# Kernel optimization log

Measured on AMD Instinct MI355X. Metric: run time of the kernel, lower is better.

Reference implementation:

```python
import jax, jax.numpy as jnp
import numpy as np

SEQ_LEN, BATCH, NUM_GROUPS, GROUP = 12, 512, 16, 32
H, E, MLP, BOTTLE, PRE = 128, 64, 1024, 1024, 512


def _pool_net(h, pos, num_groups, Wp, bp, W1, b1, W2, b2):
    # PoolHiddenNet: for each scene group, pairwise relative positions -> MLP -> max over neighbors
    B = h.shape[0]
    G = B // num_groups
    hg = h.reshape(num_groups, G, -1)          # (NG, G, H)
    pg = pos.reshape(num_groups, G, 2)         # (NG, G, 2)
    rel = pg[:, None, :, :] - pg[:, :, None, :]  # [g,i,j] = pos_j - pos_i
    emb = rel @ Wp.T + bp                      # (NG, G, G, E)
    hj = jnp.broadcast_to(hg[:, None, :, :], (num_groups, G, G, hg.shape[-1]))
    feats = jnp.concatenate([emb, hj], axis=-1)  # (NG, G, G, E+H)
    x = jax.nn.relu(feats @ W1.T + b1)         # (NG, G, G, 512)
    x = jax.nn.relu(x @ W2.T + b2)             # (NG, G, G, 1024)
    return x.max(axis=2).reshape(B, -1)        # max over neighbors j


def setup_inputs() -> dict:
    key = jax.random.key(0)
    ks = jax.random.split(key, 24)
    s = 0.05
    starts = np.arange(NUM_GROUPS, dtype=np.int64) * GROUP
    seq_start_end = jnp.asarray(np.stack([starts, starts + GROUP], axis=1))
    return {
        "last_pos": jax.random.normal(ks[0], (BATCH, 2), jnp.float32),
        "last_pos_rel": jax.random.normal(ks[1], (BATCH, 2), jnp.float32),
        "hh": jax.random.normal(ks[2], (1, BATCH, H), jnp.float32),
        "ch": jax.random.normal(ks[3], (1, BATCH, H), jnp.float32),
        "pred_traj_rel": jax.random.normal(ks[4], (SEQ_LEN, BATCH, 2), jnp.float32),
        "seq_start_end": seq_start_end,
        # LSTM (torch layout: gates ordered i,f,g,o)
        "W_ih": jax.random.normal(ks[5], (4 * H, E), jnp.float32) * s,
        "W_hh": jax.random.normal(ks[6], (4 * H, H), jnp.float32) * s,
        "b_ih": jax.random.normal(ks[7], (4 * H,), jnp.float32) * s,
        "b_hh": jax.random.normal(ks[8], (4 * H,), jnp.float32) * s,
        # spatial_embedding Linear(2, E)
        "Wse": jax.random.normal(ks[9], (E, 2), jnp.float32) * s,
        "bse": jax.random.normal(ks[10], (E,), jnp.float32) * s,
        # hidden2pos Linear(H, 2)
        "Wpos": jax.random.normal(ks[11], (2, H), jnp.float32) * s,
        "bpos": jax.random.normal(ks[12], (2,), jnp.float32) * s,
        # pool_net spatial_embedding Linear(2, E)
        "Wp": jax.random.normal(ks[13], (E, 2), jnp.float32) * s,
        "bp": jax.random.normal(ks[14], (E,), jnp.float32) * s,
        # pool_net mlp_pre_pool: [E+H, 512, BOTTLE], relu after each linear
        "W1": jax.random.normal(ks[15], (PRE, E + H), jnp.float32) * s,
        "b1": jax.random.normal(ks[16], (PRE,), jnp.float32) * s,
        "W2": jax.random.normal(ks[17], (BOTTLE, PRE), jnp.float32) * s,
        "b2": jax.random.normal(ks[18], (BOTTLE,), jnp.float32) * s,
        # decoder mlp: [H+BOTTLE, MLP, H], relu after each linear
        "Wm1": jax.random.normal(ks[19], (MLP, H + BOTTLE), jnp.float32) * s,
        "bm1": jax.random.normal(ks[20], (MLP,), jnp.float32) * s,
        "Wm2": jax.random.normal(ks[21], (H, MLP), jnp.float32) * s,
        "bm2": jax.random.normal(ks[22], (H,), jnp.float32) * s,
    }


def reference(last_pos, last_pos_rel, hh, ch, pred_traj_rel, seq_start_end,
              W_ih, W_hh, b_ih, b_hh, Wse, bse, Wpos, bpos,
              Wp, bp, W1, b1, W2, b2, Wm1, bm1, Wm2, bm2):
    num_groups = seq_start_end.shape[0]
    h0, c0 = hh[0], ch[0]
    dec_in0 = last_pos_rel @ Wse.T + bse

    def step(carry, gt_rel):
        last_pos_c, h, c, dec_in, loss = carry
        # single-layer LSTM cell (torch gate order i,f,g,o)
        gates = dec_in @ W_ih.T + b_ih + h @ W_hh.T + b_hh
        i, f, g, o = jnp.split(gates, 4, axis=-1)
        c = jax.nn.sigmoid(f) * c + jax.nn.sigmoid(i) * jnp.tanh(g)
        h = jax.nn.sigmoid(o) * jnp.tanh(c)
        rel_pos = h @ Wpos.T + bpos
        curr_pos = rel_pos + last_pos_c
        # pool every timestep + mlp back down to h_dim, replaces hidden state
        pool_h = _pool_net(h, curr_pos, num_groups, Wp, bp, W1, b1, W2, b2)
        dh = jnp.concatenate([h, pool_h], axis=1)
        dh = jax.nn.relu(dh @ Wm1.T + bm1)
        h = jax.nn.relu(dh @ Wm2.T + bm2)
        # training mode: teacher forcing + MSE loss
        loss = loss + jnp.mean((rel_pos - gt_rel) ** 2)
        dec_in = gt_rel @ Wse.T + bse
        return (curr_pos, h, c, dec_in, loss), rel_pos

    init = (last_pos, h0, c0, dec_in0, jnp.float32(0.0))
    (_, _, _, _, loss), pred_traj = jax.lax.scan(step, init, pred_traj_rel)
    return pred_traj, loss
```

## Files before the change

kernel.cpp:

```cpp
#include <hip/hip_runtime.h>
#include <math.h>

#define BATCH 512
#define NG 16
#define GSZ 32
#define H 128
#define E 64
#define PRE 512
#define BOT 1024
#define MLPD 1024
#define SEQ 12
#define AK 1152

typedef __attribute__((ext_vector_type(8))) short bf16x8;
typedef __attribute__((ext_vector_type(4))) float f32x4;

union bf8pack { ushort s[8]; uint4 v; };

__device__ __forceinline__ unsigned short f2bf(float f) {
    unsigned u = __float_as_uint(f);
    u += 0x7FFF + ((u >> 16) & 1);
    return (unsigned short)(u >> 16);
}
__device__ __forceinline__ float bf2f(unsigned short s) {
    return __uint_as_float(((unsigned)s) << 16);
}

#define GLB(p) ((const __attribute__((address_space(1))) unsigned int*)(p))
#define LDS(p) ((__attribute__((address_space(3))) unsigned int*)(p))

#define N0 (BOT * PRE)
#define N1 (MLPD * AK)
#define N2 (H * MLPD)
#define N3 (PRE * H)
#define N4 (PRE)
#define N5 (BATCH * H)
#define N5b (BATCH * H)
#define N6 (BATCH * 2)
#define N7 (512 * 128)
#define N8 (512)
#define PREP_TOT (N0 + N1 + N2 + N3 + N4 + N5 + N5b + N6 + N7 + N8 + 1)

__global__ void prep_kernel(
    const float* __restrict__ W2, const float* __restrict__ Wm1,
    const float* __restrict__ Wm2, const float* __restrict__ W1,
    const float* __restrict__ Wp, const float* __restrict__ bp, const float* __restrict__ b1,
    const float* __restrict__ ch, const float* __restrict__ hh, const float* __restrict__ last_pos,
    const float* __restrict__ Wih, const float* __restrict__ Whh,
    const float* __restrict__ bih, const float* __restrict__ bhh,
    const float* __restrict__ Wse, const float* __restrict__ bse,
    unsigned short* __restrict__ W2pk, unsigned short* __restrict__ Wm1pk,
    unsigned short* __restrict__ Wm2pk, unsigned short* __restrict__ W1pk,
    float* __restrict__ Wcx, float* __restrict__ Wcy, float* __restrict__ biash,
    float* __restrict__ cbuf, float* __restrict__ hbuf, float* __restrict__ pos,
    unsigned short* __restrict__ Whpk,
    float* __restrict__ Wx0, float* __restrict__ Wx1, float* __restrict__ bx,
    float* __restrict__ loss)
{
    long idx = (long)blockIdx.x * 256 + threadIdx.x;
    if (idx < N0) {
        int e = (int)(idx & 7);
        long u = idx >> 3;
        int lane = (int)(u & 63);
        int rest = (int)(u >> 6);
        int ksg = rest & 15, cg = rest >> 4;
        int col = cg * 16 + (lane & 15);
        int kk = ksg * 32 + (lane >> 4) * 8 + e;
        W2pk[idx] = f2bf(W2[(size_t)col * PRE + kk]);
        return;
    }
    idx -= N0;
    if (idx < N1) {
        int e = (int)(idx & 7);
        long u = idx >> 3;
        int lane = (int)(u & 63);
        long rest = u >> 6;
        int ksg = (int)(rest % 36);
        int cg = (int)(rest / 36);
        int col = cg * 16 + (lane & 15);
        int k = ksg * 32 + (lane >> 4) * 8 + e;
        Wm1pk[idx] = f2bf(Wm1[(size_t)col * AK + k]);
        return;
    }
    idx -= N1;
    if (idx < N2) {
        int e = (int)(idx & 7);
        long u = idx >> 3;
        int lane = (int)(u & 63);
        int rest = (int)(u >> 6);
        int ksg = rest & 31, cg = rest >> 5;
        int col = cg * 16 + (lane & 15);
        int k = ksg * 32 + (lane >> 4) * 8 + e;
        Wm2pk[idx] = f2bf(Wm2[(size_t)col * MLPD + k]);
        return;
    }
    idx -= N2;
    if (idx < N3) {
        int e = (int)(idx & 7);
        int u = (int)(idx >> 3);
        int l16 = u & 15, quad = (u >> 4) & 3, nt = (u >> 6) & 3, ks = (u >> 8) & 3, w = u >> 10;
        int col = w * 64 + nt * 16 + l16;
        int k = ks * 32 + quad * 8 + e;
        W1pk[idx] = f2bf(W1[col * 192 + E + k]);
        return;
    }
    idx -= N3;
    if (idx < N4) {
        int p = (int)idx;
        float sx = 0.f, sy = 0.f, sb = 0.f;
#pragma unroll 8
        for (int e = 0; e < E; ++e) {
            float w = W1[p * 192 + e];
            sx += w * Wp[e * 2 + 0];
            sy += w * Wp[e * 2 + 1];
            sb += w * bp[e];
        }
        Wcx[p] = sx; Wcy[p] = sy; biash[p] = b1[p] + sb;
        return;
    }
    idx -= N4;
    if (idx < N5) { cbuf[idx] = ch[idx]; return; }
    idx -= N5;
    if (idx < N5b) { hbuf[idx] = hh[idx]; return; }
    idx -= N5b;
    if (idx < N6) { pos[idx] = last_pos[idx]; return; }
    idx -= N6;
    if (idx < N7) {
        int e = (int)(idx & 7);
        int u = (int)(idx >> 3);
        int l16 = u & 15, quad = (u >> 4) & 3, ks = (u >> 6) & 3, w = (u >> 8) & 7, g = u >> 11;
        int col = g * 128 + w * 16 + l16;
        int k = ks * 32 + quad * 8 + e;
        Whpk[idx] = f2bf(Whh[col * H + k]);
        return;
    }
    idx -= N7;
    if (idx < N8) {
        int u = (int)idx;
        float sx = 0.f, sy = 0.f, sb = 0.f;
#pragma unroll 8
        for (int e = 0; e < E; ++e) {
            float w = Wih[u * E + e];
            sx += w * Wse[e * 2 + 0];
            sy += w * Wse[e * 2 + 1];
            sb += w * bse[e];
        }
        Wx0[u] = sx; Wx1[u] = sy; bx[u] = sb + bih[u] + bhh[u];
        return;
    }
    idx -= N8;
    if (idx == 0) *loss = 0.0f;
}

#define LROWS 16
__global__ __launch_bounds__(512) void lstm_hpart(
    int t,
    const float* __restrict__ relin, const float* __restrict__ gt,
    const unsigned short* __restrict__ Whpk,
    const float* __restrict__ Wx0, const float* __restrict__ Wx1, const float* __restrict__ bx,
    const float* __restrict__ Wpos, const float* __restrict__ bpos,
    const unsigned short* __restrict__ W1pk, const float* __restrict__ biash,
    const float* __restrict__ hbuf, float* __restrict__ cbuf,
    unsigned short* __restrict__ Abf, float* __restrict__ Hpartf,
    float* __restrict__ pos, float* __restrict__ traj, float* __restrict__ loss)
{
    constexpr int LDHB = 136;
    constexpr int LDHF = 129;
    __shared__ __align__(16) unsigned short As[LROWS * LDHB];
    __shared__ __align__(16) unsigned short hnb[LROWS * LDHB];
    __shared__ float hnf[LROWS * LDHF];
    __shared__ float lred[8];
    const int r0 = blockIdx.x * LROWS;
    const int tid = threadIdx.x;
    const int lane = tid & 63, w = tid >> 6;
    const int quad = lane >> 4, l16 = lane & 15;

    for (int idx = tid; idx < LROWS * H; idx += 512) {
        int row = idx >> 7, k = idx & 127;
        As[row * LDHB + k] = f2bf(hbuf[(size_t)(r0 + row) * H + k]);
    }
    __syncthreads();

    f32x4 acc[4];
#pragma unroll
    for (int g4 = 0; g4 < 4; ++g4) acc[g4] = (f32x4)0.f;
#pragma unroll
    for (int ks = 0; ks < 4; ++ks) {
        bf16x8 af = *(const bf16x8*)&As[l16 * LDHB + ks * 32 + quad * 8];
#pragma unroll
        for (int gate = 0; gate < 4; ++gate) {
            bf16x8 bf = *(const bf16x8*)&Whpk[((size_t)((gate * 8 + w) * 4 + ks) * 64 + lane) * 8];
            acc[gate] = __builtin_amdgcn_mfma_f32_16x16x32_bf16(af, bf, acc[gate], 0, 0, 0);
        }
    }

    {
        int u = w * 16 + l16;
        float wx0[4], wx1[4], bxv[4];
#pragma unroll
        for (int gate = 0; gate < 4; ++gate) {
            int col = gate * 128 + u;
            wx0[gate] = Wx0[col]; wx1[gate] = Wx1[col]; bxv[gate] = bx[col];
        }
#pragma unroll
        for (int r = 0; r < 4; ++r) {
            int row = quad * 4 + r;
            int b = r0 + row;
            float rx = relin[b * 2 + 0], ry = relin[b * 2 + 1];
            float i_ = acc[0][r] + rx * wx0[0] + ry * wx1[0] + bxv[0];
            float f_ = acc[1][r] + rx * wx0[1] + ry * wx1[1] + bxv[1];
            float g_ = acc[2][r] + rx * wx0[2] + ry * wx1[2] + bxv[2];
            float o_ = acc[3][r] + rx * wx0[3] + ry * wx1[3] + bxv[3];
            float ig = 1.0f / (1.0f + expf(-i_));
            float fg = 1.0f / (1.0f + expf(-f_));
            float gg = tanhf(g_);
            float og = 1.0f / (1.0f + expf(-o_));
            float c = fg * cbuf[(size_t)b * H + u] + ig * gg;
            cbuf[(size_t)b * H + u] = c;
            float h = og * tanhf(c);
            hnb[row * LDHB + u] = f2bf(h);
            hnf[row * LDHF + u] = h;
            Abf[(size_t)b * AK + u] = f2bf(h);
        }
    }
    __syncthreads();

    if (t < SEQ - 1) {
        f32x4 acc2[4];
#pragma unroll
        for (int nt = 0; nt < 4; ++nt) acc2[nt] = (f32x4)0.f;
#pragma unroll
        for (int ks = 0; ks < 4; ++ks) {
            bf16x8 af = *(const bf16x8*)&hnb[l16 * LDHB + ks * 32 + quad * 8];
#pragma unroll
            for (int nt = 0; nt < 4; ++nt) {
                bf16x8 bfr = *(const bf16x8*)&W1pk[((size_t)((w * 4 + ks) * 4 + nt) * 64 + lane) * 8];
                acc2[nt] = __builtin_amdgcn_mfma_f32_16x16x32_bf16(af, bfr, acc2[nt], 0, 0, 0);
            }
        }
#pragma unroll
        for (int nt = 0; nt < 4; ++nt) {
            int col = w * 64 + nt * 16 + l16;
            float bv = biash[col];
#pragma unroll
            for (int r = 0; r < 4; ++r) {
                int row = quad * 4 + r;
                Hpartf[(size_t)(r0 + row) * PRE + col] = acc2[nt][r] + bv;
            }
        }
    }

    {
        int row = tid >> 5, o = (tid >> 4) & 1, seg = tid & 15;
        const float* wr = Wpos + o * H + seg * 8;
        const float* hr = &hnf[row * LDHF + seg * 8];
        float acc3 = 0.f;
#pragma unroll
        for (int k = 0; k < 8; ++k) acc3 += wr[k] * hr[k];
        acc3 += __shfl_xor(acc3, 1);
        acc3 += __shfl_xor(acc3, 2);
        acc3 += __shfl_xor(acc3, 4);
        acc3 += __shfl_xor(acc3, 8);
        acc3 += bpos[o];
        int b = r0 + row;
        float d = acc3 - gt[b * 2 + o];
        if (seg == 0) {
            float lp = pos[b * 2 + o];
            pos[b * 2 + o] = acc3 + lp;
            traj[b * 2 + o] = acc3;
        }
        float part = (seg == 0) ? d * d : 0.f;
        part += __shfl_xor(part, 16);
        part += __shfl_xor(part, 32);
        if (lane == 0) lred[w] = part;
        __syncthreads();
        if (tid == 0) {
            float s = 0.f;
#pragma unroll
            for (int i = 0; i < 8; ++i) s += lred[i];
            atomicAdd(loss, s * (1.0f / 1024.0f));
        }
    }
}

template <int BM, int BN, int KW, int NW, int MODE>
__global__ __launch_bounds__(256) void gemm_splitk_pk(
    const unsigned short* __restrict__ A, int lda,
    const unsigned short* __restrict__ Bpk, int K,
    const float* __restrict__ bias,
    float* __restrict__ Cf, unsigned short* __restrict__ Cb, int ldc)
{
    constexpr int MT = BM / 16;
    constexpr int NT = BN / (16 * NW);
    __shared__ __align__(16) unsigned short As[KW * BM * 64];
    __shared__ float red[KW * BM * BN];
    int tid = threadIdx.x;
    int lane = tid & 63, w = tid >> 6;
    int kslice = w / NW, nslice = w % NW;
    int gtid = tid & (NW * 64 - 1);
    int quad = lane >> 4, l16 = lane & 15;
    int m0 = blockIdx.y * BM, n0 = blockIdx.x * BN;
    const int KC = K / KW;
    const int KSGT = K >> 5;
    const int cgbase = (n0 + nslice * (BN / NW)) >> 4;

    f32x4 acc[MT][NT];
#pragma unroll
    for (int mt = 0; mt < MT; ++mt)
#pragma unroll
        for (int nt = 0; nt < NT; ++nt) acc[mt][nt] = (f32x4)0.f;

    for (int k0 = 0; k0 < KC; k0 += 64) {
        int kb = kslice * KC + k0;
        int kgbase = kb >> 5;
#pragma unroll
        for (int u = 0; u < BM / (8 * NW); ++u) {
            int c = u * NW * 64 + gtid;
            __builtin_amdgcn_global_load_lds(
                GLB(A + (size_t)(m0 + (c >> 3)) * lda + kb + (c & 7) * 8),
                LDS(&As[kslice * BM * 64 + c * 8]), 16, 0, 0);
        }
        __syncthreads();
#pragma unroll
        for (int ks = 0; ks < 2; ++ks) {
            bf16x8 af[MT], bfr[NT];
#pragma unroll
            for (int mt = 0; mt < MT; ++mt)
                af[mt] = *(const bf16x8*)&As[kslice * BM * 64 + (mt * 16 + l16) * 64 + ks * 32 + quad * 8];
#pragma unroll
            for (int nt = 0; nt < NT; ++nt)
                bfr[nt] = *(const bf16x8*)&Bpk[((size_t)((cgbase + nt) * KSGT + kgbase + ks) * 64 + lane) * 8];
#pragma unroll
            for (int mt = 0; mt < MT; ++mt)
#pragma unroll
                for (int nt = 0; nt < NT; ++nt)
                    acc[mt][nt] = __builtin_amdgcn_mfma_f32_16x16x32_bf16(af[mt], bfr[nt], acc[mt][nt], 0, 0, 0);
        }
        __syncthreads();
    }

#pragma unroll
    for (int mt = 0; mt < MT; ++mt)
#pragma unroll
    for (int nt = 0; nt < NT; ++nt) {
#pragma unroll
        for (int r = 0; r < 4; ++r) {
            int row = mt * 16 + quad * 4 + r;
            int col = nslice * (BN / NW) + nt * 16 + l16;
            red[kslice * BM * BN + row * BN + col] = acc[mt][nt][r];
        }
    }
    __syncthreads();

#pragma unroll
    for (int o = 0; o < BM * BN / 256; ++o) {
        int e = o * 256 + tid;
        int row = e / BN, col = e % BN;
        float s = 0.f;
#pragma unroll
        for (int k = 0; k < KW; ++k) s += red[k * BM * BN + e];
        float v = fmaxf(s + bias[n0 + col], 0.f);
        if (MODE == 1) Cb[(size_t)(m0 + row) * ldc + n0 + col] = f2bf(v);
        else           Cf[(size_t)(m0 + row) * ldc + n0 + col] = v;
    }
}

__global__ __launch_bounds__(512) void pool_fused(
    const float* __restrict__ Hpartf, const float* __restrict__ pos,
    const float* __restrict__ Wcx, const float* __restrict__ Wcy,
    const unsigned short* __restrict__ W2pk,
    const float* __restrict__ b2, unsigned short* __restrict__ Abf)
{
    constexpr int BN = 512;
    constexpr int LDA = 72;
    __shared__ __align__(16) unsigned short As[128 * LDA];
    const int tid = threadIdx.x;
    const int lane = tid & 63, w = tid >> 6;
    const int quad = lane >> 4, l16 = lane & 15;
    const int n_tile = blockIdx.x, m_tile = blockIdx.y;
    const int g = m_tile >> 3, iq = m_tile & 7;
    const int n0 = n_tile * BN;

    const int brow = tid >> 2;
    const int k8 = (tid & 3) * 16;
    const int bi = iq * 4 + (brow >> 5), bj = brow & 31;
    const float rx = pos[(g * GSZ + bj) * 2 + 0] - pos[(g * GSZ + bi) * 2 + 0];
    const float ry = pos[(g * GSZ + bj) * 2 + 1] - pos[(g * GSZ + bi) * 2 + 1];
    const float* hrow = &Hpartf[(size_t)(g * GSZ + bj) * PRE];

    f32x4 acc[8][4];
#pragma unroll
    for (int mt = 0; mt < 8; ++mt)
#pragma unroll
        for (int nt = 0; nt < 4; ++nt) acc[mt][nt] = (f32x4)0.f;

    for (int k0i = 0; k0i < 8; ++k0i) {
        const int k0 = k0i * 64;
        {
            const float4* hp = (const float4*)(hrow + k0 + k8);
            const float4* wx = (const float4*)(Wcx + k0 + k8);
            const float4* wy = (const float4*)(Wcy + k0 + k8);
            bf8pack o[2];
#pragma unroll
            for (int q = 0; q < 2; ++q) {
                float4 ha = hp[q * 2], hb = hp[q * 2 + 1];
                float4 xa = wx[q * 2], xb = wx[q * 2 + 1];
                float4 ya = wy[q * 2], yb = wy[q * 2 + 1];
                o[q].s[0] = f2bf(fmaxf(ha.x + rx * xa.x + ry * ya.x, 0.f));
                o[q].s[1] = f2bf(fmaxf(ha.y + rx * xa.y + ry * ya.y, 0.f));
                o[q].s[2] = f2bf(fmaxf(ha.z + rx * xa.z + ry * ya.z, 0.f));
                o[q].s[3] = f2bf(fmaxf(ha.w + rx * xa.w + ry * ya.w, 0.f));
                o[q].s[4] = f2bf(fmaxf(hb.x + rx * xb.x + ry * yb.x, 0.f));
                o[q].s[5] = f2bf(fmaxf(hb.y + rx * xb.y + ry * yb.y, 0.f));
                o[q].s[6] = f2bf(fmaxf(hb.z + rx * xb.z + ry * yb.z, 0.f));
                o[q].s[7] = f2bf(fmaxf(hb.w + rx * xb.w + ry * yb.w, 0.f));
            }
            *(uint4*)&As[brow * LDA + k8] = o[0].v;
            *(uint4*)&As[brow * LDA + k8 + 8] = o[1].v;
        }
        __syncthreads();
#pragma unroll
        for (int ks = 0; ks < 2; ++ks) {
            bf16x8 bfr[4];
#pragma unroll
            for (int nt = 0; nt < 4; ++nt) {
                int cg = n_tile * 32 + w * 4 + nt;
                int ksg = k0i * 2 + ks;
                bfr[nt] = *(const bf16x8*)&W2pk[((size_t)(cg * 16 + ksg) * 64 + lane) * 8];
            }
#pragma unroll
            for (int mt = 0; mt < 8; ++mt) {
                bf16x8 af = *(const bf16x8*)&As[(mt * 16 + l16) * LDA + ks * 32 + quad * 8];
#pragma unroll
                for (int nt = 0; nt < 4; ++nt)
                    acc[mt][nt] = __builtin_amdgcn_mfma_f32_16x16x32_bf16(af, bfr[nt], acc[mt][nt], 0, 0, 0);
            }
        }
        __syncthreads();
    }

#pragma unroll
    for (int il = 0; il < 4; ++il)
#pragma unroll
    for (int nt = 0; nt < 4; ++nt) {
        float u = -1e30f;
#pragma unroll
        for (int p = 0; p < 2; ++p)
#pragma unroll
            for (int r = 0; r < 4; ++r) u = fmaxf(u, acc[il * 2 + p][nt][r]);
        u = fmaxf(u, __shfl_xor(u, 16));
        u = fmaxf(u, __shfl_xor(u, 32));
        if (lane < 16) {
            int col = n0 + w * 64 + nt * 16 + l16;
            int gu = m_tile * 4 + il;
            Abf[(size_t)gu * AK + H + col] = f2bf(fmaxf(u + b2[col], 0.f));
        }
    }
}

extern "C" void kernel_launch(void* const* d_in, const int* in_sizes, int n_in,
                              void* d_out, int out_size, void* d_ws, size_t ws_size,
                              hipStream_t stream)
{
    const float* last_pos     = (const float*)d_in[0];
    const float* last_pos_rel = (const float*)d_in[1];
    const float* hh           = (const float*)d_in[2];
    const float* ch           = (const float*)d_in[3];
    const float* ptr_rel      = (const float*)d_in[4];
    const float* Wih  = (const float*)d_in[6];
    const float* Whh  = (const float*)d_in[7];
    const float* bih  = (const float*)d_in[8];
    const float* bhh  = (const float*)d_in[9];
    const float* Wse  = (const float*)d_in[10];
    const float* bse  = (const float*)d_in[11];
    const float* Wpos = (const float*)d_in[12];
    const float* bpos = (const float*)d_in[13];
    const float* Wp   = (const float*)d_in[14];
    const float* bp   = (const float*)d_in[15];
    const float* W1   = (const float*)d_in[16];
    const float* b1   = (const float*)d_in[17];
    const float* W2   = (const float*)d_in[18];
    const float* b2   = (const float*)d_in[19];
    const float* Wm1  = (const float*)d_in[20];
    const float* bm1  = (const float*)d_in[21];
    const float* Wm2  = (const float*)d_in[22];
    const float* bm2  = (const float*)d_in[23];

    float* ws     = (float*)d_ws;
    float* hbuf   = ws;
    float* cbuf   = hbuf + BATCH * H;
    float* pos    = cbuf + BATCH * H;
    float* Hpartf = pos + 1024;
    float* Wcx    = Hpartf + BATCH * PRE;
    float* Wcy    = Wcx + PRE;
    float* biash  = Wcy + PRE;
    float* bx     = biash + PRE;
    float* Wx0    = bx + 512;
    float* Wx1    = Wx0 + 512;
    unsigned short* ub    = (unsigned short*)(Wx1 + 512);
    unsigned short* Abf   = ub;
    unsigned short* dhbf  = Abf + (size_t)BATCH * AK;
    unsigned short* W2pk  = dhbf + (size_t)BATCH * MLPD;
    unsigned short* Wm1pk = W2pk + (size_t)BOT * PRE;
    unsigned short* Wm2pk = Wm1pk + (size_t)MLPD * AK;
    unsigned short* W1pk  = Wm2pk + (size_t)H * MLPD;
    unsigned short* Whpk  = W1pk + (size_t)PRE * H;

    float* out  = (float*)d_out;
    float* loss = out + SEQ * BATCH * 2;

    prep_kernel<<<(PREP_TOT + 255) / 256, 256, 0, stream>>>(
        W2, Wm1, Wm2, W1, Wp, bp, b1, ch, hh, last_pos, Wih, Whh, bih, bhh, Wse, bse,
        W2pk, Wm1pk, Wm2pk, W1pk, Wcx, Wcy, biash, cbuf, hbuf, pos, Whpk, Wx0, Wx1, bx, loss);

    for (int t = 0; t < SEQ; t++) {
        const float* relin = (t == 0) ? last_pos_rel : (ptr_rel + (t - 1) * BATCH * 2);
        const float* gt = ptr_rel + t * BATCH * 2;
        lstm_hpart<<<BATCH / LROWS, 512, 0, stream>>>(t, relin, gt, Whpk, Wx0, Wx1, bx,
                                                      Wpos, bpos, W1pk, biash, hbuf, cbuf,
                                                      Abf, Hpartf, pos,
                                                      out + t * BATCH * 2, loss);
        if (t == SEQ - 1) break;
        pool_fused<<<dim3(2, 128), 512, 0, stream>>>(Hpartf, pos, Wcx, Wcy, W2pk, b2, Abf);
        gemm_splitk_pk<64, 32, 2, 2, 1><<<dim3(MLPD / 32, BATCH / 64), 256, 0, stream>>>(
            Abf, AK, Wm1pk, AK, bm1, nullptr, dhbf, MLPD);
        gemm_splitk_pk<16, 32, 4, 1, 2><<<dim3(H / 32, BATCH / 16), 256, 0, stream>>>(
            dhbf, MLPD, Wm2pk, MLPD, bm2, hbuf, nullptr, H);
    }
}
```

Baseline: 714.7 us.

## Merge per-timestep decoder kernels into one persistent kernel with grid barriers

The 45 per-timestep launches (LSTM, pooling, two MLP GEMMs) are replaced by a single persistent kernel of 256 blocks that loops over the timesteps. Stages are separated by a software grid barrier built on an atomic counter in global memory. The aim is to remove kernel launch overhead and inter-kernel gaps. In exchange, the LSTM stage now runs on only 32 of the 256 blocks while the rest wait at the barrier, and correctness depends on all 256 blocks being co-resident.

```diff
diff --git a/kernel.cpp b/kernel.cpp
--- a/kernel.cpp
+++ b/kernel.cpp
@@ -11,6 +11,7 @@
 #define MLPD 1024
 #define SEQ 12
 #define AK 1152
+#define NBLK 256
 
 typedef __attribute__((ext_vector_type(8))) short bf16x8;
 typedef __attribute__((ext_vector_type(4))) float f32x4;
@@ -21,9 +22,6 @@
     unsigned u = __float_as_uint(f);
     u += 0x7FFF + ((u >> 16) & 1);
     return (unsigned short)(u >> 16);
-}
-__device__ __forceinline__ float bf2f(unsigned short s) {
-    return __uint_as_float(((unsigned)s) << 16);
 }
 
 #define GLB(p) ((const __attribute__((address_space(1))) unsigned int*)(p))
@@ -39,7 +37,7 @@
 #define N6 (BATCH * 2)
 #define N7 (512 * 128)
 #define N8 (512)
-#define PREP_TOT (N0 + N1 + N2 + N3 + N4 + N5 + N5b + N6 + N7 + N8 + 1)
+#define PREP_TOT (N0 + N1 + N2 + N3 + N4 + N5 + N5b + N6 + N7 + N8 + 2)
 
 __global__ void prep_kernel(
     const float* __restrict__ W2, const float* __restrict__ Wm1,
@@ -55,7 +53,7 @@
     float* __restrict__ cbuf, float* __restrict__ hbuf, float* __restrict__ pos,
     unsigned short* __restrict__ Whpk,
     float* __restrict__ Wx0, float* __restrict__ Wx1, float* __restrict__ bx,
-    float* __restrict__ loss)
+    float* __restrict__ loss, unsigned* __restrict__ barcnt)
 {
     long idx = (long)blockIdx.x * 256 + threadIdx.x;
     if (idx < N0) {
@@ -149,312 +147,382 @@
         return;
     }
     idx -= N8;
-    if (idx == 0) *loss = 0.0f;
+    if (idx == 0) { *loss = 0.0f; return; }
+    if (idx == 1) { *barcnt = 0u; return; }
 }
 
+__device__ __forceinline__ void gsync(unsigned* cnt, unsigned target) {
+    __syncthreads();
+    if (threadIdx.x == 0) {
+        __threadfence();
+        atomicAdd(cnt, 1u);
+        while (__hip_atomic_load(cnt, __ATOMIC_RELAXED, __HIP_MEMORY_SCOPE_AGENT) < target)
+            __builtin_amdgcn_s_sleep(16);
+        __threadfence();
+    }
+    __syncthreads();
+}
+
 #define LROWS 16
-__global__ __launch_bounds__(512) void lstm_hpart(
-    int t,
-    const float* __restrict__ relin, const float* __restrict__ gt,
+__global__ __launch_bounds__(512, 2) void decoder_persistent(
+    const float* __restrict__ last_pos_rel, const float* __restrict__ ptr_rel,
     const unsigned short* __restrict__ Whpk,
     const float* __restrict__ Wx0, const float* __restrict__ Wx1, const float* __restrict__ bx,
     const float* __restrict__ Wpos, const float* __restrict__ bpos,
     const unsigned short* __restrict__ W1pk, const float* __restrict__ biash,
-    const float* __restrict__ hbuf, float* __restrict__ cbuf,
+    const float* __restrict__ Wcx, const float* __restrict__ Wcy,
+    const unsigned short* __restrict__ W2pk, const float* __restrict__ b2,
+    const unsigned short* __restrict__ Wm1pk, const float* __restrict__ bm1,
+    const unsigned short* __restrict__ Wm2pk, const float* __restrict__ bm2,
+    float* __restrict__ hbuf, float* __restrict__ cbuf,
     unsigned short* __restrict__ Abf, float* __restrict__ Hpartf,
-    float* __restrict__ pos, float* __restrict__ traj, float* __restrict__ loss)
+    unsigned short* __restrict__ dhbf,
+    float* __restrict__ pos, float* __restrict__ out, float* __restrict__ loss,
+    unsigned* __restrict__ barcnt)
 {
-    constexpr int LDHB = 136;
-    constexpr int LDHF = 129;
-    __shared__ __align__(16) unsigned short As[LROWS * LDHB];
-    __shared__ __align__(16) unsigned short hnb[LROWS * LDHB];
-    __shared__ float hnf[LROWS * LDHF];
-    __shared__ float lred[8];
-    const int r0 = blockIdx.x * LROWS;
-    const int tid = threadIdx.x;
+    __shared__ __align__(16) unsigned char smem[32768];
+    const int blk = blockIdx.x, tid = threadIdx.x;
     const int lane = tid & 63, w = tid >> 6;
     const int quad = lane >> 4, l16 = lane & 15;
-
-    for (int idx = tid; idx < LROWS * H; idx += 512) {
-        int row = idx >> 7, k = idx & 127;
-        As[row * LDHB + k] = f2bf(hbuf[(size_t)(r0 + row) * H + k]);
-    }
-    __syncthreads();
-
-    f32x4 acc[4];
-#pragma unroll
-    for (int g4 = 0; g4 < 4; ++g4) acc[g4] = (f32x4)0.f;
-#pragma unroll
-    for (int ks = 0; ks < 4; ++ks) {
-        bf16x8 af = *(const bf16x8*)&As[l16 * LDHB + ks * 32 + quad * 8];
-#pragma unroll
-        for (int gate = 0; gate < 4; ++gate) {
-            bf16x8 bf = *(const bf16x8*)&Whpk[((size_t)((gate * 8 + w) * 4 + ks) * 64 + lane) * 8];
-            acc[gate] = __builtin_amdgcn_mfma_f32_16x16x32_bf16(af, bf, acc[gate], 0, 0, 0);
+    unsigned phase = 0;
+
+    for (int t = 0; t < SEQ; ++t) {
+        if (blk < 32) {
+            constexpr int LDHB = 136;
+            constexpr int LDHF = 129;
+            unsigned short* As = (unsigned short*)smem;
+            unsigned short* hnb = As + LROWS * LDHB;
+            float* hnf = (float*)(hnb + LROWS * LDHB);
+            float* lred = hnf + LROWS * LDHF;
+            const int r0 = blk * LROWS;
+            const float* relin = (t == 0) ? last_pos_rel : (ptr_rel + (t - 1) * BATCH * 2);
+            const float* gt = ptr_rel + t * BATCH * 2;
+            float* traj = out + t * BATCH * 2;
+
+            for (int e2 = tid; e2 < LROWS * H; e2 += 512) {
+                int row = e2 >> 7, k = e2 & 127;
+                As[row * LDHB + k] = f2bf(hbuf[(size_t)(r0 + row) * H + k]);
+            }
+            __syncthreads();
+
+            f32x4 acc[4];
+#pragma unroll
+            for (int g4 = 0; g4 < 4; ++g4) acc[g4] = (f32x4)0.f;
+#pragma unroll
+            for (int ks = 0; ks < 4; ++ks) {
+                bf16x8 af = *(const bf16x8*)&As[l16 * LDHB + ks * 32 + quad * 8];
+#pragma unroll
+                for (int gate = 0; gate < 4; ++gate) {
+                    bf16x8 bf = *(const bf16x8*)&Whpk[((size_t)((gate * 8 + w) * 4 + ks) * 64 + lane) * 8];
+                    acc[gate] = __builtin_amdgcn_mfma_f32_16x16x32_bf16(af, bf, acc[gate], 0, 0, 0);
+                }
+            }
+
+            {
+                int u = w * 16 + l16;
+                float wx0[4], wx1[4], bxv[4];
+#pragma unroll
+                for (int gate = 0; gate < 4; ++gate) {
+                    int col = gate * 128 + u;
+                    wx0[gate] = Wx0[col]; wx1[gate] = Wx1[col]; bxv[gate] = bx[col];
+                }
+#pragma unroll
+                for (int r = 0; r < 4; ++r) {
+                    int row = quad * 4 + r;
+                    int b = r0 + row;
+                    float rx = relin[b * 2 + 0], ry = relin[b * 2 + 1];
+                    float i_ = acc[0][r] + rx * wx0[0] + ry * wx1[0] + bxv[0];
+                    float f_ = acc[1][r] + rx * wx0[1] + ry * wx1[1] + bxv[1];
+                    float g_ = acc[2][r] + rx * wx0[2] + ry * wx1[2] + bxv[2];
+                    float o_ = acc[3][r] + rx * wx0[3] + ry * wx1[3] + bxv[3];
+                    float ig = 1.0f / (1.0f + expf(-i_));
+                    float fg = 1.0f / (1.0f + expf(-f_));
+                    float gg = tanhf(g_);
+                    float og = 1.0f / (1.0f + expf(-o_));
+                    float c = fg * cbuf[(size_t)b * H + u] + ig * gg;
+                    cbuf[(size_t)b * H + u] = c;
+                    float h = og * tanhf(c);
+                    hnb[row * LDHB + u] = f2bf(h);
+                    hnf[row * LDHF + u] = h;
+                    Abf[(size_t)b * AK + u] = f2bf(h);
+                }
+            }
+            __syncthreads();
+
+            if (t < SEQ - 1) {
+                f32x4 acc2[4];
+#pragma unroll
+                for (int nt = 0; nt < 4; ++nt) acc2[nt] = (f32x4)0.f;
+#pragma unroll
+                for (int ks = 0; ks < 4; ++ks) {
+                    bf16x8 af = *(const bf16x8*)&hnb[l16 * LDHB + ks * 32 + quad * 8];
+#pragma unroll
+                    for (int nt = 0; nt < 4; ++nt) {
+                        bf16x8 bfr = *(const bf16x8*)&W1pk[((size_t)((w * 4 + ks) * 4 + nt) * 64 + lane) * 8];
+                        acc2[nt] = __builtin_amdgcn_mfma_f32_16x16x32_bf16(af, bfr, acc2[nt], 0, 0, 0);
+                    }
+                }
+#pragma unroll
+                for (int nt = 0; nt < 4; ++nt) {
+                    int col = w * 64 + nt * 16 + l16;
+                    float bv = biash[col];
+#pragma unroll
+                    for (int r = 0; r < 4; ++r) {
+                        int row = quad * 4 + r;
+                        Hpartf[(size_t)(r0 + row) * PRE + col] = acc2[nt][r] + bv;
+                    }
+                }
+            }
+
+            {
+                int row = tid >> 5, o = (tid >> 4) & 1, seg = tid & 15;
+                const float* wr = Wpos + o * H + seg * 8;
+                const float* hr = &hnf[row * LDHF + seg * 8];
+                float acc3 = 0.f;
+#pragma unroll
+                for (int k = 0; k < 8; ++k) acc3 += wr[k] * hr[k];
+                acc3 += __shfl_xor(acc3, 1);
+                acc3 += __shfl_xor(acc3, 2);
+                acc3 += __shfl_xor(acc3, 4);
+                acc3 += __shfl_xor(acc3, 8);
+                acc3 += bpos[o];
+                int b = r0 + row;
+                float d = acc3 - gt[b * 2 + o];
+                if (seg == 0) {
+                    float lp = pos[b * 2 + o];
+                    pos[b * 2 + o] = acc3 + lp;
+                    traj[b * 2 + o] = acc3;
+                }
+                float part = (seg == 0) ? d * d : 0.f;
+                part += __shfl_xor(part, 16);
+                part += __shfl_xor(part, 32);
+                if (lane == 0) lred[w] = part;
+                __syncthreads();
+                if (tid == 0) {
+                    float s = 0.f;
+#pragma unroll
+                    for (int i = 0; i < 8; ++i) s += lred[i];
+                    atomicAdd(loss, s * (1.0f / 1024.0f));
+                }
+            }
         }
-    }
-
-    {
-        int u = w * 16 + l16;
-        float wx0[4], wx1[4], bxv[4];
-#pragma unroll
-        for (int gate = 0; gate < 4; ++gate) {
-            int col = gate * 128 + u;
-            wx0[gate] = Wx0[col]; wx1[gate] = Wx1[col]; bxv[gate] = bx[col];
+        if (t == SEQ - 1) break;
+        ++phase; gsync(barcnt, phase * NBLK);
+
+        {
+            constexpr int LDA = 72;
+            unsigned short* AsP = (unsigned short*)smem;
+            const int n_tile = blk & 1, m_tile = blk >> 1;
+            const int g = m_tile >> 3, iq = m_tile & 7;
+            const int n0 = n_tile * 512;
+            const int brow = tid >> 2;
+            const int k8 = (tid & 3) * 16;
+            const int bi = iq * 4 + (brow >> 5), bj = brow & 31;
+            const float rx = pos[(g * GSZ + bj) * 2 + 0] - pos[(g * GSZ + bi) * 2 + 0];
+            const float ry = pos[(g * GSZ + bj) * 2 + 1] - pos[(g * GSZ + bi) * 2 + 1];
+            const float* hrow = &Hpartf[(size_t)(g * GSZ + bj) * PRE];
+
+            f32x4 acc[8][4];
+#pragma unroll
+            for (int mt = 0; mt < 8; ++mt)
+#pragma unroll
+                for (int nt = 0; nt < 4; ++nt) acc[mt][nt] = (f32x4)0.f;
+
+            for (int k0i = 0; k0i < 8; ++k0i) {
+                const int k0 = k0i * 64;
+                {
+                    const float4* hp = (const float4*)(hrow + k0 + k8);
+                    const float4* wx = (const float4*)(Wcx + k0 + k8);
+                    const float4* wy = (const float4*)(Wcy + k0 + k8);
+                    bf8pack o[2];
+#pragma unroll
+                    for (int q = 0; q < 2; ++q) {
+                        float4 ha = hp[q * 2], hb = hp[q * 2 + 1];
+                        float4 xa = wx[q * 2], xb = wx[q * 2 + 1];
+                        float4 ya = wy[q * 2], yb = wy[q * 2 + 1];
+                        o[q].s[0] = f2bf(fmaxf(ha.x + rx * xa.x + ry * ya.x, 0.f));
+                        o[q].s[1] = f2bf(fmaxf(ha.y + rx * xa.y + ry * ya.y, 0.f));
+                        o[q].s[2] = f2bf(fmaxf(ha.z + rx * xa.z + ry * ya.z, 0.f));
+                        o[q].s[3] = f2bf(fmaxf(ha.w + rx * xa.w + ry * ya.w, 0.f));
+                        o[q].s[4] = f2bf(fmaxf(hb.x + rx * xb.x + ry * yb.x, 0.f));
+                        o[q].s[5] = f2bf(fmaxf(hb.y + rx * xb.y + ry * yb.y, 0.f));
+                        o[q].s[6] = f2bf(fmaxf(hb.z + rx * xb.z + ry * yb.z, 0.f));
+                        o[q].s[7] = f2bf(fmaxf(hb.w + rx * xb.w + ry * yb.w, 0.f));
+                    }
+                    *(uint4*)&AsP[brow * LDA + k8] = o[0].v;
+                    *(uint4*)&AsP[brow * LDA + k8 + 8] = o[1].v;
+                }
+                __syncthreads();
+#pragma unroll
+                for (int ks = 0; ks < 2; ++ks) {
+                    bf16x8 bfr[4];
+#pragma unroll
+                    for (int nt = 0; nt < 4; ++nt) {
+                        int cg = n_tile * 32 + w * 4 + nt;
+                        int ksg = k0i * 2 + ks;
+                        bfr[nt] = *(const bf16x8*)&W2pk[((size_t)(cg * 16 + ksg) * 64 + lane) * 8];
+                    }
+#pragma unroll
+                    for (int mt = 0; mt < 8; ++mt) {
+                        bf16x8 af = *(const bf16x8*)&AsP[(mt * 16 + l16) * LDA + ks * 32 + quad * 8];
+#pragma unroll
+                        for (int nt = 0; nt < 4; ++nt)
+                            acc[mt][nt] = __builtin_amdgcn_mfma_f32_16x16x32_bf16(af, bfr[nt], acc[mt][nt], 0, 0, 0);
+                    }
+                }
+                __syncthreads();
+            }
+
+#pragma unroll
+            for (int il = 0; il < 4; ++il)
+#pragma unroll
+            for (int nt = 0; nt < 4; ++nt) {
+                float u = -1e30f;
+#pragma unroll
+                for (int p = 0; p < 2; ++p)
+#pragma unroll
+                    for (int r = 0; r < 4; ++r) u = fmaxf(u, acc[il * 2 + p][nt][r]);
+                u = fmaxf(u, __shfl_xor(u, 16));
+                u = fmaxf(u, __shfl_xor(u, 32));
+                if (lane < 16) {
+                    int col = n0 + w * 64 + nt * 16 + l16;
+                    int gu = m_tile * 4 + il;
+                    Abf[(size_t)gu * AK + H + col] = f2bf(fmaxf(u + b2[col], 0.f));
+                }
+            }
         }
-#pragma unroll
-        for (int r = 0; r < 4; ++r) {
-            int row = quad * 4 + r;
-            int b = r0 + row;
-            float rx = relin[b * 2 + 0], ry = relin[b * 2 + 1];
-            float i_ = acc[0][r] + rx * wx0[0] + ry * wx1[0] + bxv[0];
-            float f_ = acc[1][r] + rx * wx0[1] + ry * wx1[1] + bxv[1];
-            float g_ = acc[2][r] + rx * wx0[2] + ry * wx1[2] + bxv[2];
-            float o_ = acc[3][r] + rx * wx0[3] + ry * wx1[3] + bxv[3];
-            float ig = 1.0f / (1.0f + expf(-i_));
-            float fg = 1.0f / (1.0f + expf(-f_));
-            float gg = tanhf(g_);
-            float og = 1.0f / (1.0f + expf(-o_));
-            float c = fg * cbuf[(size_t)b * H + u] + ig * gg;
-            cbuf[(size_t)b * H + u] = c;
-            float h = og * tanhf(c);
-            hnb[row * LDHB + u] = f2bf(h);
-            hnf[row * LDHF + u] = h;
-            Abf[(size_t)b * AK + u] = f2bf(h);
+        ++phase; gsync(barcnt, phase * NBLK);
+
+        {
+            const int n0 = (blk & 31) * 32, m0 = (blk >> 5) * 64;
+            const bool act = tid < 256;
+            unsigned short* AsM = (unsigned short*)smem;
+            float* red = (float*)(smem + 16384);
+            const int w4 = (tid >> 6) & 3;
+            const int kslice = w4 >> 1, nslice = w4 & 1;
+            const int gtid = tid & 127;
+            const int cgbase = n0 / 16 + nslice;
+
+            f32x4 acc[4];
+#pragma unroll
+            for (int mt = 0; mt < 4; ++mt) acc[mt] = (f32x4)0.f;
+
+            for (int k0 = 0; k0 < 576; k0 += 64) {
+                int kb = kslice * 576 + k0;
+                int kgbase = kb >> 5;
+                if (act) {
+#pragma unroll
+                    for (int u = 0; u < 4; ++u) {
+                        int c = u * 128 + gtid;
+                        __builtin_amdgcn_global_load_lds(
+                            GLB(Abf + (size_t)(m0 + (c >> 3)) * AK + kb + (c & 7) * 8),
+                            LDS(&AsM[kslice * 4096 + c * 8]), 16, 0, 0);
+                    }
+                }
+                __syncthreads();
+                if (act) {
+#pragma unroll
+                    for (int ks = 0; ks < 2; ++ks) {
+                        bf16x8 af[4];
+#pragma unroll
+                        for (int mt = 0; mt < 4; ++mt)
+                            af[mt] = *(const bf16x8*)&AsM[kslice * 4096 + (mt * 16 + l16) * 64 + ks * 32 + quad * 8];
+                        bf16x8 bfr = *(const bf16x8*)&Wm1pk[((size_t)(cgbase * 36 + kgbase + ks) * 64 + lane) * 8];
+#pragma unroll
+                        for (int mt = 0; mt < 4; ++mt)
+                            acc[mt] = __builtin_amdgcn_mfma_f32_16x16x32_bf16(af[mt], bfr, acc[mt], 0, 0, 0);
+                    }
+                }
+                __syncthreads();
+            }
+
+            if (act) {
+#pragma unroll
+                for (int mt = 0; mt < 4; ++mt)
+#pragma unroll
+                for (int r = 0; r < 4; ++r) {
+                    int row = mt * 16 + quad * 4 + r;
+                    int col = nslice * 16 + l16;
+                    red[kslice * 2048 + row * 32 + col] = acc[mt][r];
+                }
+            }
+            __syncthreads();
+            if (act) {
+#pragma unroll
+                for (int o = 0; o < 8; ++o) {
+                    int e = o * 256 + tid;
+                    int row = e >> 5, col = e & 31;
+                    float s = red[e] + red[2048 + e];
+                    float v = fmaxf(s + bm1[n0 + col], 0.f);
+                    dhbf[(size_t)(m0 + row) * MLPD + n0 + col] = f2bf(v);
+                }
+            }
         }
-    }
-    __syncthreads();
-
-    if (t < SEQ - 1) {
-        f32x4 acc2[4];
-#pragma unroll
-        for (int nt = 0; nt < 4; ++nt) acc2[nt] = (f32x4)0.f;
-#pragma unroll
-        for (int ks = 0; ks < 4; ++ks) {
-            bf16x8 af = *(const bf16x8*)&hnb[l16 * LDHB + ks * 32 + quad * 8];
-#pragma unroll
-            for (int nt = 0; nt < 4; ++nt) {
-                bf16x8 bfr = *(const bf16x8*)&W1pk[((size_t)((w * 4 + ks) * 4 + nt) * 64 + lane) * 8];
-                acc2[nt] = __builtin_amdgcn_mfma_f32_16x16x32_bf16(af, bfr, acc2[nt], 0, 0, 0);
+        ++phase; gsync(barcnt, phase * NBLK);
+
+        if (blk < 128) {
+            const int n0 = (blk & 3) * 32, m0 = (blk >> 2) * 16;
+            const bool act = tid < 256;
+            unsigned short* As2 = (unsigned short*)smem;
+            float* red2 = (float*)(smem + 8192);
+            const int w4 = (tid >> 6) & 3;
+            const int gtid2 = tid & 63;
+            const int cgbase = n0 >> 4;
+
+            f32x4 acc[2];
+#pragma unroll
+            for (int nt = 0; nt < 2; ++nt) acc[nt] = (f32x4)0.f;
+
+            for (int k0 = 0; k0 < 256; k0 += 64) {
+                int kb = w4 * 256 + k0;
+                int kgbase = kb >> 5;
+                if (act) {
+#pragma unroll
+                    for (int u = 0; u < 2; ++u) {
+                        int c = u * 64 + gtid2;
+                        __builtin_amdgcn_global_load_lds(
+                            GLB(dhbf + (size_t)(m0 + (c >> 3)) * MLPD + kb + (c & 7) * 8),
+                            LDS(&As2[w4 * 1024 + c * 8]), 16, 0, 0);
+                    }
+                }
+                __syncthreads();
+                if (act) {
+#pragma unroll
+                    for (int ks = 0; ks < 2; ++ks) {
+                        bf16x8 af = *(const bf16x8*)&As2[w4 * 1024 + l16 * 64 + ks * 32 + quad * 8];
+#pragma unroll
+                        for (int nt = 0; nt < 2; ++nt) {
+                            bf16x8 bfr = *(const bf16x8*)&Wm2pk[((size_t)((cgbase + nt) * 32 + kgbase + ks) * 64 + lane) * 8];
+                            acc[nt] = __builtin_amdgcn_mfma_f32_16x16x32_bf16(af, bfr, acc[nt], 0, 0, 0);
+                        }
+                    }
+                }
+                __syncthreads();
+            }
+
+            if (act) {
+#pragma unroll
+                for (int nt = 0; nt < 2; ++nt)
+#pragma unroll
+                for (int r = 0; r < 4; ++r) {
+                    int row = quad * 4 + r;
+                    int col = nt * 16 + l16;
+                    red2[w4 * 512 + row * 32 + col] = acc[nt][r];
+                }
+            }
+            __syncthreads();
+            if (act) {
+#pragma unroll
+                for (int o = 0; o < 2; ++o) {
+                    int e = o * 256 + tid;
+                    int row = e >> 5, col = e & 31;
+                    float s = red2[e] + red2[512 + e] + red2[1024 + e] + red2[1536 + e];
+                    float v = fmaxf(s + bm2[n0 + col], 0.f);
+                    hbuf[(size_t)(m0 + row) * H + n0 + col] = v;
+                }
             }
         }
-#pragma unroll
-        for (int nt = 0; nt < 4; ++nt) {
-            int col = w * 64 + nt * 16 + l16;
-            float bv = biash[col];
-#pragma unroll
-            for (int r = 0; r < 4; ++r) {
-                int row = quad * 4 + r;
-                Hpartf[(size_t)(r0 + row) * PRE + col] = acc2[nt][r] + bv;
-            }
-        }
-    }
-
-    {
-        int row = tid >> 5, o = (tid >> 4) & 1, seg = tid & 15;
-        const float* wr = Wpos + o * H + seg * 8;
-        const float* hr = &hnf[row * LDHF + seg * 8];
-        float acc3 = 0.f;
-#pragma unroll
-        for (int k = 0; k < 8; ++k) acc3 += wr[k] * hr[k];
-        acc3 += __shfl_xor(acc3, 1);
-        acc3 += __shfl_xor(acc3, 2);
-        acc3 += __shfl_xor(acc3, 4);
-        acc3 += __shfl_xor(acc3, 8);
-        acc3 += bpos[o];
-        int b = r0 + row;
-        float d = acc3 - gt[b * 2 + o];
-        if (seg == 0) {
-            float lp = pos[b * 2 + o];
-            pos[b * 2 + o] = acc3 + lp;
-            traj[b * 2 + o] = acc3;
-        }
-        float part = (seg == 0) ? d * d : 0.f;
-        part += __shfl_xor(part, 16);
-        part += __shfl_xor(part, 32);
-        if (lane == 0) lred[w] = part;
-        __syncthreads();
-        if (tid == 0) {
-            float s = 0.f;
-#pragma unroll
-            for (int i = 0; i < 8; ++i) s += lred[i];
-            atomicAdd(loss, s * (1.0f / 1024.0f));
-        }
-    }
-}
-
-template <int BM, int BN, int KW, int NW, int MODE>
-__global__ __launch_bounds__(256) void gemm_splitk_pk(
-    const unsigned short* __restrict__ A, int lda,
-    const unsigned short* __restrict__ Bpk, int K,
-    const float* __restrict__ bias,
-    float* __restrict__ Cf, unsigned short* __restrict__ Cb, int ldc)
-{
-    constexpr int MT = BM / 16;
-    constexpr int NT = BN / (16 * NW);
-    __shared__ __align__(16) unsigned short As[KW * BM * 64];
-    __shared__ float red[KW * BM * BN];
-    int tid = threadIdx.x;
-    int lane = tid & 63, w = tid >> 6;
-    int kslice = w / NW, nslice = w % NW;
-    int gtid = tid & (NW * 64 - 1);
-    int quad = lane >> 4, l16 = lane & 15;
-    int m0 = blockIdx.y * BM, n0 = blockIdx.x * BN;
-    const int KC = K / KW;
-    const int KSGT = K >> 5;
-    const int cgbase = (n0 + nslice * (BN / NW)) >> 4;
-
-    f32x4 acc[MT][NT];
-#pragma unroll
-    for (int mt = 0; mt < MT; ++mt)
-#pragma unroll
-        for (int nt = 0; nt < NT; ++nt) acc[mt][nt] = (f32x4)0.f;
-
-    for (int k0 = 0; k0 < KC; k0 += 64) {
-        int kb = kslice * KC + k0;
-        int kgbase = kb >> 5;
-#pragma unroll
-        for (int u = 0; u < BM / (8 * NW); ++u) {
-            int c = u * NW * 64 + gtid;
-            __builtin_amdgcn_global_load_lds(
-                GLB(A + (size_t)(m0 + (c >> 3)) * lda + kb + (c & 7) * 8),
-                LDS(&As[kslice * BM * 64 + c * 8]), 16, 0, 0);
-        }
-        __syncthreads();
-#pragma unroll
-        for (int ks = 0; ks < 2; ++ks) {
-            bf16x8 af[MT], bfr[NT];
-#pragma unroll
-            for (int mt = 0; mt < MT; ++mt)
-                af[mt] = *(const bf16x8*)&As[kslice * BM * 64 + (mt * 16 + l16) * 64 + ks * 32 + quad * 8];
-#pragma unroll
-            for (int nt = 0; nt < NT; ++nt)
-                bfr[nt] = *(const bf16x8*)&Bpk[((size_t)((cgbase + nt) * KSGT + kgbase + ks) * 64 + lane) * 8];
-#pragma unroll
-            for (int mt = 0; mt < MT; ++mt)
-#pragma unroll
-                for (int nt = 0; nt < NT; ++nt)
-                    acc[mt][nt] = __builtin_amdgcn_mfma_f32_16x16x32_bf16(af[mt], bfr[nt], acc[mt][nt], 0, 0, 0);
-        }
-        __syncthreads();
-    }
-
-#pragma unroll
-    for (int mt = 0; mt < MT; ++mt)
-#pragma unroll
-    for (int nt = 0; nt < NT; ++nt) {
-#pragma unroll
-        for (int r = 0; r < 4; ++r) {
-            int row = mt * 16 + quad * 4 + r;
-            int col = nslice * (BN / NW) + nt * 16 + l16;
-            red[kslice * BM * BN + row * BN + col] = acc[mt][nt][r];
-        }
-    }
-    __syncthreads();
-
-#pragma unroll
-    for (int o = 0; o < BM * BN / 256; ++o) {
-        int e = o * 256 + tid;
-        int row = e / BN, col = e % BN;
-        float s = 0.f;
-#pragma unroll
-        for (int k = 0; k < KW; ++k) s += red[k * BM * BN + e];
-        float v = fmaxf(s + bias[n0 + col], 0.f);
-        if (MODE == 1) Cb[(size_t)(m0 + row) * ldc + n0 + col] = f2bf(v);
-        else           Cf[(size_t)(m0 + row) * ldc + n0 + col] = v;
-    }
-}
-
-__global__ __launch_bounds__(512) void pool_fused(
-    const float* __restrict__ Hpartf, const float* __restrict__ pos,
-    const float* __restrict__ Wcx, const float* __restrict__ Wcy,
-    const unsigned short* __restrict__ W2pk,
-    const float* __restrict__ b2, unsigned short* __restrict__ Abf)
-{
-    constexpr int BN = 512;
-    constexpr int LDA = 72;
-    __shared__ __align__(16) unsigned short As[128 * LDA];
-    const int tid = threadIdx.x;
-    const int lane = tid & 63, w = tid >> 6;
-    const int quad = lane >> 4, l16 = lane & 15;
-    const int n_tile = blockIdx.x, m_tile = blockIdx.y;
-    const int g = m_tile >> 3, iq = m_tile & 7;
-    const int n0 = n_tile * BN;
-
-    const int brow = tid >> 2;
-    const int k8 = (tid & 3) * 16;
-    const int bi = iq * 4 + (brow >> 5), bj = brow & 31;
-    const float rx = pos[(g * GSZ + bj) * 2 + 0] - pos[(g * GSZ + bi) * 2 + 0];
-    const float ry = pos[(g * GSZ + bj) * 2 + 1] - pos[(g * GSZ + bi) * 2 + 1];
-    const float* hrow = &Hpartf[(size_t)(g * GSZ + bj) * PRE];
-
-    f32x4 acc[8][4];
-#pragma unroll
-    for (int mt = 0; mt < 8; ++mt)
-#pragma unroll
-        for (int nt = 0; nt < 4; ++nt) acc[mt][nt] = (f32x4)0.f;
-
-    for (int k0i = 0; k0i < 8; ++k0i) {
-        const int k0 = k0i * 64;
-        {
-            const float4* hp = (const float4*)(hrow + k0 + k8);
-            const float4* wx = (const float4*)(Wcx + k0 + k8);
-            const float4* wy = (const float4*)(Wcy + k0 + k8);
-            bf8pack o[2];
-#pragma unroll
-            for (int q = 0; q < 2; ++q) {
-                float4 ha = hp[q * 2], hb = hp[q * 2 + 1];
-                float4 xa = wx[q * 2], xb = wx[q * 2 + 1];
-                float4 ya = wy[q * 2], yb = wy[q * 2 + 1];
-                o[q].s[0] = f2bf(fmaxf(ha.x + rx * xa.x + ry * ya.x, 0.f));
-                o[q].s[1] = f2bf(fmaxf(ha.y + rx * xa.y + ry * ya.y, 0.f));
-                o[q].s[2] = f2bf(fmaxf(ha.z + rx * xa.z + ry * ya.z, 0.f));
-                o[q].s[3] = f2bf(fmaxf(ha.w + rx * xa.w + ry * ya.w, 0.f));
-                o[q].s[4] = f2bf(fmaxf(hb.x + rx * xb.x + ry * yb.x, 0.f));
-                o[q].s[5] = f2bf(fmaxf(hb.y + rx * xb.y + ry * yb.y, 0.f));
-                o[q].s[6] = f2bf(fmaxf(hb.z + rx * xb.z + ry * yb.z, 0.f));
-                o[q].s[7] = f2bf(fmaxf(hb.w + rx * xb.w + ry * yb.w, 0.f));
-            }
-            *(uint4*)&As[brow * LDA + k8] = o[0].v;
-            *(uint4*)&As[brow * LDA + k8 + 8] = o[1].v;
-        }
-        __syncthreads();
-#pragma unroll
-        for (int ks = 0; ks < 2; ++ks) {
-            bf16x8 bfr[4];
-#pragma unroll
-            for (int nt = 0; nt < 4; ++nt) {
-                int cg = n_tile * 32 + w * 4 + nt;
-                int ksg = k0i * 2 + ks;
-                bfr[nt] = *(const bf16x8*)&W2pk[((size_t)(cg * 16 + ksg) * 64 + lane) * 8];
-            }
-#pragma unroll
-            for (int mt = 0; mt < 8; ++mt) {
-                bf16x8 af = *(const bf16x8*)&As[(mt * 16 + l16) * LDA + ks * 32 + quad * 8];
-#pragma unroll
-                for (int nt = 0; nt < 4; ++nt)
-                    acc[mt][nt] = __builtin_amdgcn_mfma_f32_16x16x32_bf16(af, bfr[nt], acc[mt][nt], 0, 0, 0);
-            }
-        }
-        __syncthreads();
-    }
-
-#pragma unroll
-    for (int il = 0; il < 4; ++il)
-#pragma unroll
-    for (int nt = 0; nt < 4; ++nt) {
-        float u = -1e30f;
-#pragma unroll
-        for (int p = 0; p < 2; ++p)
-#pragma unroll
-            for (int r = 0; r < 4; ++r) u = fmaxf(u, acc[il * 2 + p][nt][r]);
-        u = fmaxf(u, __shfl_xor(u, 16));
-        u = fmaxf(u, __shfl_xor(u, 32));
-        if (lane < 16) {
-            int col = n0 + w * 64 + nt * 16 + l16;
-            int gu = m_tile * 4 + il;
-            Abf[(size_t)gu * AK + H + col] = f2bf(fmaxf(u + b2[col], 0.f));
-        }
+        ++phase; gsync(barcnt, phase * NBLK);
     }
 }
 
@@ -505,26 +573,18 @@
     unsigned short* Wm2pk = Wm1pk + (size_t)MLPD * AK;
     unsigned short* W1pk  = Wm2pk + (size_t)H * MLPD;
     unsigned short* Whpk  = W1pk + (size_t)PRE * H;
+    unsigned* barcnt      = (unsigned*)(Whpk + (size_t)512 * 128);
 
     float* out  = (float*)d_out;
     float* loss = out + SEQ * BATCH * 2;
 
     prep_kernel<<<(PREP_TOT + 255) / 256, 256, 0, stream>>>(
         W2, Wm1, Wm2, W1, Wp, bp, b1, ch, hh, last_pos, Wih, Whh, bih, bhh, Wse, bse,
-        W2pk, Wm1pk, Wm2pk, W1pk, Wcx, Wcy, biash, cbuf, hbuf, pos, Whpk, Wx0, Wx1, bx, loss);
-
-    for (int t = 0; t < SEQ; t++) {
-        const float* relin = (t == 0) ? last_pos_rel : (ptr_rel + (t - 1) * BATCH * 2);
-        const float* gt = ptr_rel + t * BATCH * 2;
-        lstm_hpart<<<BATCH / LROWS, 512, 0, stream>>>(t, relin, gt, Whpk, Wx0, Wx1, bx,
-                                                      Wpos, bpos, W1pk, biash, hbuf, cbuf,
-                                                      Abf, Hpartf, pos,
-                                                      out + t * BATCH * 2, loss);
-        if (t == SEQ - 1) break;
-        pool_fused<<<dim3(2, 128), 512, 0, stream>>>(Hpartf, pos, Wcx, Wcy, W2pk, b2, Abf);
-        gemm_splitk_pk<64, 32, 2, 2, 1><<<dim3(MLPD / 32, BATCH / 64), 256, 0, stream>>>(
-            Abf, AK, Wm1pk, AK, bm1, nullptr, dhbf, MLPD);
-        gemm_splitk_pk<16, 32, 4, 1, 2><<<dim3(H / 32, BATCH / 16), 256, 0, stream>>>(
-            dhbf, MLPD, Wm2pk, MLPD, bm2, hbuf, nullptr, H);
-    }
+        W2pk, Wm1pk, Wm2pk, W1pk, Wcx, Wcy, biash, cbuf, hbuf, pos, Whpk, Wx0, Wx1, bx,
+        loss, barcnt);
+
+    decoder_persistent<<<NBLK, 512, 0, stream>>>(
+        last_pos_rel, ptr_rel, Whpk, Wx0, Wx1, bx, Wpos, bpos, W1pk, biash,
+        Wcx, Wcy, W2pk, b2, Wm1pk, bm1, Wm2pk, bm2,
+        hbuf, cbuf, Abf, Hpartf, dhbf, pos, out, loss, barcnt);
 }
```

After: 1.805 ms. 2.53x slower.
